# Optimization experiments

Measured on AMD Instinct MI355X. Metric: run time of the kernel, lower is better.

Reference implementation:

```python
import jax, jax.numpy as jnp
import numpy as np

K, N, MEM_D = 512, 4096, 64


def setup_inputs() -> dict:
    key = jax.random.key(0)
    k1, k2, k3, k4 = jax.random.split(key, 4)
    # event counts per location/time (torch code uses raw observations; rand in [0,1) keeps log-lik finite)
    obs = jax.random.uniform(k1, (K, N), jnp.float32)
    extobs = jax.random.normal(k2, (K, N), jnp.float32)
    beta = jnp.asarray(2.0, jnp.float32)  # torch.Tensor([2]) scalar rate parameter
    alpha = jax.random.uniform(k3, (K, K), jnp.float32, 0.0, 0.01)
    gamma = jax.random.uniform(k4, (K, MEM_D), jnp.float32, 0.0, 0.01)
    return {"obs": obs, "extobs": extobs, "beta": beta, "alpha": alpha, "gamma": gamma}


def reference(obs, extobs, beta, alpha, gamma):
    Kk, Nn = obs.shape
    d = gamma.shape[1]
    # mu is derived from obs exactly as in __init__ (not a trainable parameter)
    mu = obs.mean(axis=1) / 10.0 + 0.01  # [K]

    t = jnp.arange(Nn)
    diff = t[:, None] - t[None, :]  # [N, N], diff[t, j] = t - j
    # strict lower-triangular exponential decay kernel: D[t, j] = beta * exp(-(t-j)*beta) for j < t
    # clamp diff before exp so masked entries never produce inf (keeps vjp NaN-free)
    safe = jnp.maximum(diff, 1).astype(jnp.float32)
    Dmat = jnp.where(diff > 0, beta * jnp.exp(-safe * beta), 0.0)  # [N, N]

    # lam1[k, t] = sum_{k'} alpha[k, k'] * sum_{j < t} obs[k', j] * beta * exp(-(t-j)*beta)
    lam1 = alpha @ (obs @ Dmat.T)  # [K, N]

    # lam2[k, t] = sum_i extobs[k, t-d+i] * gamma[k, i]  (only when t >= d, else 0)
    # depthwise 1D cross-correlation with left zero-padding of d, then mask t < d
    x = extobs[None]            # [1, K, N]
    w = gamma[:, None, :]       # [K, 1, d]
    lam2 = jax.lax.conv_general_dilated(
        x, w, window_strides=(1,), padding=[(d, 0)],
        dimension_numbers=("NCH", "OIH", "NCH"), feature_group_count=Kk,
    )[0, :, :Nn]                # [K, N]
    lam2 = jnp.where(t[None, :] >= d, lam2, 0.0)

    lams = jax.nn.softplus(mu[:, None] + lam1 + lam2)  # [K, N]
    loglik = (obs * jnp.log(lams) - lams).sum()
    return (loglik, lams)
```

## Files before the change

### kernel.cpp

```cpp
#include <hip/hip_runtime.h>
#include <math.h>

#define KDIM 512
#define NDIM 4096
#define MEMD 64
#define WTAPS 16
#define SEG 1024
#define NSEG (NDIM / SEG)
#define NPART (KDIM * NSEG)

#define GBM 64
#define GBN 64
#define GBK 64

typedef short bf16x8 __attribute__((ext_vector_type(8)));
typedef float f32x4 __attribute__((ext_vector_type(4)));

#define GLOAD_LDS16(g, l) __builtin_amdgcn_global_load_lds( \
    (const __attribute__((address_space(1))) unsigned int*)(g), \
    (__attribute__((address_space(3))) unsigned int*)(l), 16, 0, 0)

__device__ __forceinline__ void bsplit(float a, ushort& hi, ushort& lo) {
    uint u = __float_as_uint(a);
    uint h = (u + 0x7FFFu + ((u >> 16) & 1u)) >> 16;
    hi = (ushort)h;
    float hf = __uint_as_float(h << 16);
    float r = a - hf;
    uint u2 = __float_as_uint(r);
    lo = (ushort)((u2 + 0x7FFFu + ((u2 >> 16) & 1u)) >> 16);
}

__device__ __forceinline__ float block_reduce_256(float v, float* sbuf) {
    #pragma unroll
    for (int off = 32; off > 0; off >>= 1) v += __shfl_down(v, off, 64);
    int lane = threadIdx.x & 63, wid = threadIdx.x >> 6;
    if (lane == 0) sbuf[wid] = v;
    __syncthreads();
    float tot = sbuf[0] + sbuf[1] + sbuf[2] + sbuf[3];
    __syncthreads();
    return tot;
}

__device__ __forceinline__ double block_reduce_256d(double v, double* dbuf) {
    #pragma unroll
    for (int off = 32; off > 0; off >>= 1) v += __shfl_down(v, off, 64);
    int lane = threadIdx.x & 63, wid = threadIdx.x >> 6;
    if (lane == 0) dbuf[wid] = v;
    __syncthreads();
    double tot = dbuf[0] + dbuf[1] + dbuf[2] + dbuf[3];
    __syncthreads();
    return tot;
}

__global__ __launch_bounds__(256) void conv_kernel(
    const float* __restrict__ B, const float* __restrict__ A,
    ushort* __restrict__ Bthi, ushort* __restrict__ Btlo,
    ushort* __restrict__ Ahi, ushort* __restrict__ Alo,
    float* __restrict__ mu) {
    __shared__ float s[32][33];
    int b = blockIdx.x, tid = threadIdx.x;
    if (b < 2048) {
        int n0 = (b & 127) * 32, k0 = (b >> 7) * 32;
        int r = tid >> 5, c = tid & 31;
        #pragma unroll
        for (int i = 0; i < 4; ++i)
            s[r + i * 8][c] = B[(size_t)(k0 + r + i * 8) * NDIM + n0 + c];
        __syncthreads();
        int rr = tid >> 4, cc = (tid & 15) * 2;
        #pragma unroll
        for (int i = 0; i < 2; ++i) {
            int n = rr + i * 16;
            float a0 = s[cc][n], a1 = s[cc + 1][n];
            ushort h0, l0, h1, l1;
            bsplit(a0, h0, l0); bsplit(a1, h1, l1);
            size_t o = (size_t)(n0 + n) * KDIM + k0 + cc;
            *(ushort2*)&Bthi[o] = make_ushort2(h0, h1);
            *(ushort2*)&Btlo[o] = make_ushort2(l0, l1);
        }
    } else if (b < 2176) {
        int ab = b - 2048;
        int g = ab * 256 + tid;
        const float4* src = (const float4*)A;
        #pragma unroll
        for (int i = 0; i < 2; ++i) {
            float4 v = src[g * 2 + i];
            ushort4 h, l;
            bsplit(v.x, h.x, l.x); bsplit(v.y, h.y, l.y);
            bsplit(v.z, h.z, l.z); bsplit(v.w, h.w, l.w);
            *(ushort4*)&Ahi[(size_t)g * 8 + i * 4] = h;
            *(ushort4*)&Alo[(size_t)g * 8 + i * 4] = l;
        }
    } else {
        int k = b - 2176;
        const float* row = B + (size_t)k * NDIM;
        float ss = 0.f;
        for (int j = tid; j < NDIM; j += 256) ss += row[j];
        float tot = block_reduce_256(ss, &s[0][0]);
        if (tid == 0) mu[k] = tot / (float)NDIM / 10.0f + 0.01f;
    }
}

__global__ __launch_bounds__(256) void mfma_gemm(
    const ushort* __restrict__ Ahi, const ushort* __restrict__ Alo,
    const ushort* __restrict__ Bthi, const ushort* __restrict__ Btlo,
    float* __restrict__ C) {
    __shared__ __align__(16) ushort Asm[2][GBM * GBK];
    __shared__ __align__(16) ushort Bsm[2][GBN * GBK];
    int tid = threadIdx.x;
    int m0 = blockIdx.y * GBM, n0 = blockIdx.x * GBN;
    int l = tid & 63, w = tid >> 6;
    int wm = w >> 1, wn = w & 1;
    int lr = l & 15, lk = l >> 4;

    f32x4 acc[2][2];
    #pragma unroll
    for (int i = 0; i < 2; ++i)
        #pragma unroll
        for (int j = 0; j < 2; ++j) acc[i][j] = (f32x4){0.f, 0.f, 0.f, 0.f};

    for (int c0 = 0; c0 < KDIM; c0 += GBK) {
        #pragma unroll
        for (int i = 0; i < 4; ++i) {
            int c = tid + i * 256;
            int plane = c >> 9, q = c & 511;
            int row = q >> 3, kc = (q & 7) ^ (row & 7);
            const ushort* sa = (plane ? Alo : Ahi) + (size_t)(m0 + row) * KDIM + c0 + kc * 8;
            GLOAD_LDS16(sa, (char*)&Asm[0][0] + c * 16);
            const ushort* sb = (plane ? Btlo : Bthi) + (size_t)(n0 + row) * KDIM + c0 + kc * 8;
            GLOAD_LDS16(sb, (char*)&Bsm[0][0] + c * 16);
        }
        __syncthreads();
        bf16x8 ah[2][2], al[2][2], bh[2][2], bl[2][2];
        #pragma unroll
        for (int mf = 0; mf < 2; ++mf)
            #pragma unroll
            for (int s = 0; s < 2; ++s) {
                int ra = wm * 32 + mf * 16 + lr;
                int offa = ra * 128 + (((s * 64) + lk * 16) ^ ((ra & 7) << 4));
                ah[mf][s] = *(const bf16x8*)((const char*)&Asm[0][0] + offa);
                al[mf][s] = *(const bf16x8*)((const char*)&Asm[1][0] + offa);
                int rb = wn * 32 + mf * 16 + lr;
                int offb = rb * 128 + (((s * 64) + lk * 16) ^ ((rb & 7) << 4));
                bh[mf][s] = *(const bf16x8*)((const char*)&Bsm[0][0] + offb);
                bl[mf][s] = *(const bf16x8*)((const char*)&Bsm[1][0] + offb);
            }
        #pragma unroll
        for (int s = 0; s < 2; ++s)
            #pragma unroll
            for (int mf = 0; mf < 2; ++mf)
                #pragma unroll
                for (int nf = 0; nf < 2; ++nf) {
                    acc[mf][nf] = __builtin_amdgcn_mfma_f32_16x16x32_bf16(ah[mf][s], bh[nf][s], acc[mf][nf], 0, 0, 0);
                    acc[mf][nf] = __builtin_amdgcn_mfma_f32_16x16x32_bf16(ah[mf][s], bl[nf][s], acc[mf][nf], 0, 0, 0);
                    acc[mf][nf] = __builtin_amdgcn_mfma_f32_16x16x32_bf16(al[mf][s], bh[nf][s], acc[mf][nf], 0, 0, 0);
                }
        __syncthreads();
    }
    #pragma unroll
    for (int mf = 0; mf < 2; ++mf)
        #pragma unroll
        for (int nf = 0; nf < 2; ++nf)
            #pragma unroll
            for (int j = 0; j < 4; ++j) {
                int rm = m0 + wm * 32 + mf * 16 + lk * 4 + j;
                int cn = n0 + wn * 32 + nf * 16 + lr;
                C[(size_t)rm * NDIM + cn] = acc[mf][nf][j];
            }
}

__global__ __launch_bounds__(256) void final_kernel(
    const float* __restrict__ T, const float* __restrict__ obs,
    const float* __restrict__ extobs, const float* __restrict__ gamma,
    const float* __restrict__ beta_p, const float* __restrict__ mu,
    float* __restrict__ lams_out, double* __restrict__ partials) {
    __shared__ float Ts[SEG + 16];
    __shared__ float Es[SEG + 64];
    __shared__ float Os[SEG];
    __shared__ float Gs[MEMD];
    __shared__ float Wt[WTAPS];
    __shared__ double dbuf[4];

    int b = blockIdx.x, tid = threadIdx.x;
    int k = b >> 2, s = b & 3;
    float beta = *beta_p;
    float muk = mu[k];

    const float4* gT = (const float4*)(T + (size_t)k * NDIM);
    const float4* gE = (const float4*)(extobs + (size_t)k * NDIM);
    const float4* gO = (const float4*)(obs + (size_t)k * NDIM);
    float4 z = make_float4(0.f, 0.f, 0.f, 0.f);

    {
        for (int i = tid; i < 260; i += 256) {
            int gi = s * 256 - 4 + i;
            ((float4*)Ts)[i] = (gi >= 0) ? gT[gi] : z;
        }
        for (int i = tid; i < 272; i += 256) {
            int gi = s * 256 - 16 + i;
            ((float4*)Es)[i] = (gi >= 0) ? gE[gi] : z;
        }
        ((float4*)Os)[tid] = gO[s * 256 + tid];
        if (tid < MEMD) Gs[tid] = gamma[(size_t)k * MEMD + tid];
        if (tid >= 64 && tid < 64 + WTAPS) {
            int m = tid - 63;
            Wt[m - 1] = beta * expf(-beta * (float)m);
        }
    }
    __syncthreads();

    int t_loc = tid * 4;
    int t = s * SEG + t_loc;
    float win[20];
    float l1[4] = {0.f, 0.f, 0.f, 0.f};
    float l2[4] = {0.f, 0.f, 0.f, 0.f};

    #pragma unroll
    for (int c = 0; c < 5; ++c) *(float4*)&win[c * 4] = *(const float4*)&Ts[t_loc + c * 4];
    #pragma unroll
    for (int m = 1; m <= WTAPS; ++m) {
        float wm = Wt[m - 1];
        #pragma unroll
        for (int j = 0; j < 4; ++j) l1[j] = fmaf(wm, win[16 + j - m], l1[j]);
    }

    #pragma unroll
    for (int c4 = 0; c4 < 4; ++c4) {
        #pragma unroll
        for (int c = 0; c < 5; ++c)
            *(float4*)&win[c * 4] = *(const float4*)&Es[t_loc + c4 * 16 + c * 4];
        #pragma unroll
        for (int i = 0; i < 16; ++i) {
            float g = Gs[c4 * 16 + i];
            #pragma unroll
            for (int j = 0; j < 4; ++j) l2[j] = fmaf(g, win[i + j], l2[j]);
        }
    }
    if (t < MEMD) { l2[0] = 0.f; l2[1] = 0.f; l2[2] = 0.f; l2[3] = 0.f; }

    float4 o = ((const float4*)Os)[tid];
    float oo[4] = {o.x, o.y, o.z, o.w};
    double part = 0.0;
    f32x4 sv;
    #pragma unroll
    for (int j = 0; j < 4; ++j) {
        float x = muk + l1[j] + l2[j];
        float sp = fmaxf(x, 0.f) + log1pf(expf(-fabsf(x)));
        sv[j] = sp;
        part += (double)(oo[j] * logf(sp) - sp);
    }
    *(f32x4*)&lams_out[(size_t)k * NDIM + t] = sv;

    double dtot = block_reduce_256d(part, dbuf);
    if (tid == 0) partials[b] = dtot;
}

__global__ __launch_bounds__(256) void reduce_kernel(const double* __restrict__ partials,
                                                     float* __restrict__ out) {
    __shared__ double dbuf[4];
    double v = 0.0;
    for (int j = threadIdx.x; j < NPART; j += 256) v += partials[j];
    double tot = block_reduce_256d(v, dbuf);
    if (threadIdx.x == 0) out[0] = (float)tot;
}

extern "C" void kernel_launch(void* const* d_in, const int* in_sizes, int n_in,
                              void* d_out, int out_size, void* d_ws, size_t ws_size,
                              hipStream_t stream) {
    const float* obs    = (const float*)d_in[0];
    const float* extobs = (const float*)d_in[1];
    const float* beta   = (const float*)d_in[2];
    const float* alpha  = (const float*)d_in[3];
    const float* gamma  = (const float*)d_in[4];
    float* out = (float*)d_out;

    char* ws = (char*)d_ws;
    float*  T        = (float*)(ws);
    ushort* Bthi     = (ushort*)(ws + (8u << 20));
    ushort* Btlo     = (ushort*)(ws + (12u << 20));
    ushort* Ahi      = (ushort*)(ws + (16u << 20));
    ushort* Alo      = (ushort*)(ws + (16u << 20) + (512u << 10));
    double* partials = (double*)(ws + (17u << 20));
    float* mu        = (float*)(ws + (17u << 20) + (32u << 10));

    conv_kernel<<<2048 + 128 + 512, 256, 0, stream>>>(obs, alpha, Bthi, Btlo,
                                                      Ahi, Alo, mu);
    mfma_gemm<<<dim3(NDIM / GBN, KDIM / GBM), 256, 0, stream>>>(Ahi, Alo, Bthi, Btlo, T);
    final_kernel<<<NPART, 256, 0, stream>>>(T, obs, extobs, gamma, beta, mu,
                                            out + 1, partials);
    reduce_kernel<<<1, 256, 0, stream>>>(partials, out);
}
```

Baseline: 116.0 us.

## Double-buffer GEMM LDS tiles and widen transpose-split tiles to 64x64

The MFMA GEMM now keeps two LDS stages and issues the global-to-LDS load for the next K-chunk before computing on the current one, so memory latency can overlap with MFMA work. The obs transpose/bf16-split kernel moves from 32x32 to 64x64 tiles, reading with float4 and writing 16-byte vectors of eight packed bf16 values instead of ushort2 pairs. This doubles GEMM LDS use to 64KB per block, which may reduce occupancy. There is also a possible hazard: the next stage's async LDS loads are waited on only by the end-of-iteration barrier, with no explicit vmcnt wait.

```diff
diff --git a/kernel.cpp b/kernel.cpp
--- a/kernel.cpp
+++ b/kernel.cpp
@@ -57,28 +57,32 @@
     ushort* __restrict__ Bthi, ushort* __restrict__ Btlo,
     ushort* __restrict__ Ahi, ushort* __restrict__ Alo,
     float* __restrict__ mu) {
-    __shared__ float s[32][33];
+    __shared__ float s[64][65];
     int b = blockIdx.x, tid = threadIdx.x;
-    if (b < 2048) {
-        int n0 = (b & 127) * 32, k0 = (b >> 7) * 32;
-        int r = tid >> 5, c = tid & 31;
-        #pragma unroll
-        for (int i = 0; i < 4; ++i)
-            s[r + i * 8][c] = B[(size_t)(k0 + r + i * 8) * NDIM + n0 + c];
+    if (b < 512) {
+        int n0 = (b & 63) * 64, k0 = (b >> 6) * 64;
+        #pragma unroll
+        for (int i = 0; i < 4; ++i) {
+            int idx = i * 256 + tid;
+            int row = idx >> 4, c4 = idx & 15;
+            float4 v = *(const float4*)&B[(size_t)(k0 + row) * NDIM + n0 + c4 * 4];
+            s[row][c4 * 4 + 0] = v.x; s[row][c4 * 4 + 1] = v.y;
+            s[row][c4 * 4 + 2] = v.z; s[row][c4 * 4 + 3] = v.w;
+        }
         __syncthreads();
-        int rr = tid >> 4, cc = (tid & 15) * 2;
         #pragma unroll
         for (int i = 0; i < 2; ++i) {
-            int n = rr + i * 16;
-            float a0 = s[cc][n], a1 = s[cc + 1][n];
-            ushort h0, l0, h1, l1;
-            bsplit(a0, h0, l0); bsplit(a1, h1, l1);
-            size_t o = (size_t)(n0 + n) * KDIM + k0 + cc;
-            *(ushort2*)&Bthi[o] = make_ushort2(h0, h1);
-            *(ushort2*)&Btlo[o] = make_ushort2(l0, l1);
-        }
-    } else if (b < 2176) {
-        int ab = b - 2048;
+            int idx = i * 256 + tid;
+            int n = idx >> 3, k8 = idx & 7;
+            ushort hs[8], ls[8];
+            #pragma unroll
+            for (int j = 0; j < 8; ++j) bsplit(s[k8 * 8 + j][n], hs[j], ls[j]);
+            size_t o = (size_t)(n0 + n) * KDIM + k0 + k8 * 8;
+            *(uint4*)&Bthi[o] = *(const uint4*)hs;
+            *(uint4*)&Btlo[o] = *(const uint4*)ls;
+        }
+    } else if (b < 640) {
+        int ab = b - 512;
         int g = ab * 256 + tid;
         const float4* src = (const float4*)A;
         #pragma unroll
@@ -91,7 +95,7 @@
             *(ushort4*)&Alo[(size_t)g * 8 + i * 4] = l;
         }
     } else {
-        int k = b - 2176;
+        int k = b - 640;
         const float* row = B + (size_t)k * NDIM;
         float ss = 0.f;
         for (int j = tid; j < NDIM; j += 256) ss += row[j];
@@ -104,8 +108,8 @@
     const ushort* __restrict__ Ahi, const ushort* __restrict__ Alo,
     const ushort* __restrict__ Bthi, const ushort* __restrict__ Btlo,
     float* __restrict__ C) {
-    __shared__ __align__(16) ushort Asm[2][GBM * GBK];
-    __shared__ __align__(16) ushort Bsm[2][GBN * GBK];
+    __shared__ __align__(16) ushort Asm[2][2][GBM * GBK];
+    __shared__ __align__(16) ushort Bsm[2][2][GBN * GBK];
     int tid = threadIdx.x;
     int m0 = blockIdx.y * GBM, n0 = blockIdx.x * GBN;
     int l = tid & 63, w = tid >> 6;
@@ -118,18 +122,25 @@
         #pragma unroll
         for (int j = 0; j < 2; ++j) acc[i][j] = (f32x4){0.f, 0.f, 0.f, 0.f};
 
-    for (int c0 = 0; c0 < KDIM; c0 += GBK) {
-        #pragma unroll
-        for (int i = 0; i < 4; ++i) {
-            int c = tid + i * 256;
-            int plane = c >> 9, q = c & 511;
-            int row = q >> 3, kc = (q & 7) ^ (row & 7);
-            const ushort* sa = (plane ? Alo : Ahi) + (size_t)(m0 + row) * KDIM + c0 + kc * 8;
-            GLOAD_LDS16(sa, (char*)&Asm[0][0] + c * 16);
-            const ushort* sb = (plane ? Btlo : Bthi) + (size_t)(n0 + row) * KDIM + c0 + kc * 8;
-            GLOAD_LDS16(sb, (char*)&Bsm[0][0] + c * 16);
-        }
-        __syncthreads();
+#define STAGE(bb, c0)                                                              \
+    _Pragma("unroll")                                                              \
+    for (int i_ = 0; i_ < 4; ++i_) {                                               \
+        int c_ = tid + i_ * 256;                                                   \
+        int plane_ = c_ >> 9, q_ = c_ & 511;                                       \
+        int row_ = q_ >> 3, kc_ = (q_ & 7) ^ (row_ & 7);                           \
+        const ushort* sa_ = (plane_ ? Alo : Ahi) + (size_t)(m0 + row_) * KDIM + (c0) + kc_ * 8; \
+        GLOAD_LDS16(sa_, (char*)&Asm[bb][0][0] + c_ * 16);                         \
+        const ushort* sb_ = (plane_ ? Btlo : Bthi) + (size_t)(n0 + row_) * KDIM + (c0) + kc_ * 8; \
+        GLOAD_LDS16(sb_, (char*)&Bsm[bb][0][0] + c_ * 16);                         \
+    }
+
+    STAGE(0, 0);
+    __syncthreads();
+
+    for (int t = 0; t < 8; ++t) {
+        int cur = t & 1;
+        if (t < 7) { STAGE(cur ^ 1, (t + 1) * GBK); }
+
         bf16x8 ah[2][2], al[2][2], bh[2][2], bl[2][2];
         #pragma unroll
         for (int mf = 0; mf < 2; ++mf)
@@ -137,12 +148,12 @@
             for (int s = 0; s < 2; ++s) {
                 int ra = wm * 32 + mf * 16 + lr;
                 int offa = ra * 128 + (((s * 64) + lk * 16) ^ ((ra & 7) << 4));
-                ah[mf][s] = *(const bf16x8*)((const char*)&Asm[0][0] + offa);
-                al[mf][s] = *(const bf16x8*)((const char*)&Asm[1][0] + offa);
+                ah[mf][s] = *(const bf16x8*)((const char*)&Asm[cur][0][0] + offa);
+                al[mf][s] = *(const bf16x8*)((const char*)&Asm[cur][1][0] + offa);
                 int rb = wn * 32 + mf * 16 + lr;
                 int offb = rb * 128 + (((s * 64) + lk * 16) ^ ((rb & 7) << 4));
-                bh[mf][s] = *(const bf16x8*)((const char*)&Bsm[0][0] + offb);
-                bl[mf][s] = *(const bf16x8*)((const char*)&Bsm[1][0] + offb);
+                bh[mf][s] = *(const bf16x8*)((const char*)&Bsm[cur][0][0] + offb);
+                bl[mf][s] = *(const bf16x8*)((const char*)&Bsm[cur][1][0] + offb);
             }
         #pragma unroll
         for (int s = 0; s < 2; ++s)
@@ -156,6 +167,8 @@
                 }
         __syncthreads();
     }
+#undef STAGE
+
     #pragma unroll
     for (int mf = 0; mf < 2; ++mf)
         #pragma unroll
@@ -282,8 +295,8 @@
     double* partials = (double*)(ws + (17u << 20));
     float* mu        = (float*)(ws + (17u << 20) + (32u << 10));
 
-    conv_kernel<<<2048 + 128 + 512, 256, 0, stream>>>(obs, alpha, Bthi, Btlo,
-                                                      Ahi, Alo, mu);
+    conv_kernel<<<512 + 128 + 512, 256, 0, stream>>>(obs, alpha, Bthi, Btlo,
+                                                     Ahi, Alo, mu);
     mfma_gemm<<<dim3(NDIM / GBN, KDIM / GBM), 256, 0, stream>>>(Ahi, Alo, Bthi, Btlo, T);
     final_kernel<<<NPART, 256, 0, stream>>>(T, obs, extobs, gamma, beta, mu,
                                             out + 1, partials);
```

Measured after the change: 115.0 us. Within noise of the previous version (-0.9%).
